# Optimization experiments

Hardware: AMD Instinct MI355X
Metric: run time of the kernel (lower is better)

Reference implementation:

```python
import jax, jax.numpy as jnp
import numpy as np

B, T, D, H, L = 128, 512, 512, 512, 256


def setup_inputs() -> dict:
    key = jax.random.key(0)
    ks = jax.random.split(key, 7)
    lim = 1.0 / np.sqrt(H)
    u = lambda k, shape, lo: jax.random.uniform(k, shape, jnp.float32, -lo, lo)
    x = jax.random.normal(ks[0], (B, T, D), dtype=jnp.float32)
    Wih = u(ks[1], (3 * H, D), lim)
    Whh = u(ks[2], (3 * H, H), lim)
    b = u(ks[3], (3 * H,), lim)
    bn = u(ks[4], (H,), lim)
    lim_l = 1.0 / np.sqrt(H)
    Wlin = u(ks[5], (2 * L, H), lim_l)
    blin = u(ks[6], (2 * L,), lim_l)
    return {"x": x, "Wih": Wih, "Whh": Whh, "b": b, "bn": bn, "Wlin": Wlin, "blin": blin}


def reference(x, Wih, Whh, b, bn, Wlin, blin):
    # x: (B, T, D). Batched GRU recurrence over time via lax.scan.
    def step(h, xt):
        ig = xt @ Wih.T + b           # (B, 3H)
        hg = h @ Whh.T                # (B, 3H)
        ir, iz, inn = jnp.split(ig, 3, axis=-1)
        hr, hz, hn = jnp.split(hg, 3, axis=-1)
        r = jax.nn.sigmoid(ir + hr)
        z = jax.nn.sigmoid(iz + hz)
        n = jnp.tanh(inn + r * (hn + bn))
        h_new = (1.0 - z) * n + z * h
        return h_new, None

    xs = jnp.swapaxes(x, 0, 1)        # (T, B, D)
    h0 = jnp.zeros((x.shape[0], Whh.shape[1]), dtype=x.dtype)
    h_final, _ = jax.lax.scan(step, h0, xs)
    out = h_final @ Wlin.T + blin     # (B, 2L)
    mu, logvar = jnp.split(out, 2, axis=-1)
    return (mu, logvar)
```

## Files before the change

kernel.cpp:

```cpp
#include <hip/hip_runtime.h>
#include <stdint.h>


typedef short short8 __attribute__((ext_vector_type(8)));
typedef float f32x4 __attribute__((ext_vector_type(4)));
typedef int int4v __attribute__((ext_vector_type(4)));

#define NB 128
#define NT 512
#define ND 512
#define NH 512
#define NG 1536
#define HSLOT (NB * NH)

__device__ __forceinline__ unsigned short f2bf(float f) {
  union { float f; unsigned u; } v; v.f = f;
  unsigned r = v.u + 0x7fffu + ((v.u >> 16) & 1u);
  return (unsigned short)(r >> 16);
}
__device__ __forceinline__ float bf2f(unsigned short u) {
  union { unsigned u; float f; } v; v.u = ((unsigned)u) << 16; return v.f;
}
__device__ __forceinline__ float sigmoid_f(float x) {
  float e = __builtin_amdgcn_exp2f(-1.4426950408889634f * x);
  return __builtin_amdgcn_rcpf(1.0f + e);
}
__device__ __forceinline__ float tanh_f(float x) {
  float e = __builtin_amdgcn_exp2f(2.8853900817779268f * x);
  return 1.0f - 2.0f * __builtin_amdgcn_rcpf(1.0f + e);
}
__device__ __forceinline__ short8 pack8(float4 a, float4 b) {
  short8 s;
  s[0] = (short)f2bf(a.x); s[1] = (short)f2bf(a.y);
  s[2] = (short)f2bf(a.z); s[3] = (short)f2bf(a.w);
  s[4] = (short)f2bf(b.x); s[5] = (short)f2bf(b.y);
  s[6] = (short)f2bf(b.z); s[7] = (short)f2bf(b.w);
  return s;
}

__device__ __forceinline__ int4v load16_s(const unsigned short* p) {
  int4v v;
  asm volatile("global_load_dwordx4 %0, %1, off sc0 sc1\n\t"
               "s_waitcnt vmcnt(0)"
               : "=v"(v) : "v"(p) : "memory");
  return v;
}

__device__ __forceinline__ void load16x2_s(const unsigned short* p0,
                                           const unsigned short* p1,
                                           int4v* v0, int4v* v1) {
  asm volatile(
      "global_load_dwordx4 %0, %2, off sc0 sc1\n\t"
      "global_load_dwordx4 %1, %3, off sc0 sc1\n\t"
      "s_waitcnt vmcnt(0)"
      : "=&v"(*v0), "=&v"(*v1) : "v"(p0), "v"(p1) : "memory");
}

__device__ __forceinline__ void store8_nd(unsigned short* p, unsigned long long v) {
  asm volatile("global_store_dwordx2 %0, %1, off sc0 sc1"
               :: "v"(p), "v"(v) : "memory");
}

__device__ __forceinline__ unsigned pkmax(unsigned a, unsigned b) {
  unsigned d;
  asm("v_pk_max_u16 %0, %1, %2" : "=v"(d) : "v"(a), "v"(b));
  return d;
}
__device__ __forceinline__ bool has_sent(int4v v) {
  unsigned m = pkmax(pkmax((unsigned)v[0], (unsigned)v[1]),
                     pkmax((unsigned)v[2], (unsigned)v[3]));
  return ((m & 0xFFFFu) == 0xFFFFu) || ((m >> 16) == 0xFFFFu);
}

__global__ __launch_bounds__(256) void ig_gemm(
    const float* __restrict__ x, const float* __restrict__ Wih,
    const float* __restrict__ bias, unsigned short* __restrict__ IG) {
  __shared__ unsigned short As[128 * 40];
  __shared__ unsigned short Bs[128 * 40];
  const int tid = threadIdx.x;
  const int bn = blockIdx.x, bm = blockIdx.y;
  const int lane = tid & 63, w = tid >> 6;
  const int wm = w >> 1, wn = w & 1;
  const int l15 = lane & 15, q = lane >> 4;

  f32x4 acc[4][4] = {};

  for (int kt = 0; kt < 16; ++kt) {
    __syncthreads();
#pragma unroll
    for (int j = 0; j < 4; ++j) {
      int fi = tid + 256 * j;
      int row = fi >> 3, kq = fi & 7;
      float4 v = *(const float4*)(x + (size_t)(bm * 128 + row) * ND + kt * 32 + kq * 4);
      ushort4 s = {f2bf(v.x), f2bf(v.y), f2bf(v.z), f2bf(v.w)};
      *(ushort4*)&As[row * 40 + kq * 4] = s;
    }
#pragma unroll
    for (int j = 0; j < 4; ++j) {
      int fi = tid + 256 * j;
      int row = fi >> 3, kq = fi & 7;
      float4 v = *(const float4*)(Wih + (size_t)(bn * 128 + row) * ND + kt * 32 + kq * 4);
      ushort4 s = {f2bf(v.x), f2bf(v.y), f2bf(v.z), f2bf(v.w)};
      *(ushort4*)&Bs[row * 40 + kq * 4] = s;
    }
    __syncthreads();

    short8 af[4], bf[4];
#pragma unroll
    for (int tm = 0; tm < 4; ++tm)
      af[tm] = *(const short8*)&As[(wm * 64 + tm * 16 + l15) * 40 + q * 8];
#pragma unroll
    for (int tn = 0; tn < 4; ++tn)
      bf[tn] = *(const short8*)&Bs[(wn * 64 + tn * 16 + l15) * 40 + q * 8];
#pragma unroll
    for (int tm = 0; tm < 4; ++tm)
#pragma unroll
      for (int tn = 0; tn < 4; ++tn)
        acc[tm][tn] = __builtin_amdgcn_mfma_f32_16x16x32_bf16(af[tm], bf[tn], acc[tm][tn], 0, 0, 0);
  }

#pragma unroll
  for (int tm = 0; tm < 4; ++tm) {
#pragma unroll
    for (int tn = 0; tn < 4; ++tn) {
      int col = bn * 128 + wn * 64 + tn * 16 + l15;
      float bb = bias[col];
#pragma unroll
      for (int i = 0; i < 4; ++i) {
        int row = bm * 128 + wm * 64 + tm * 16 + q * 4 + i;
        IG[(size_t)row * NG + col] = f2bf(acc[tm][tn][i] + bb);
      }
    }
  }
}

template <bool USE_IG>
__global__ __launch_bounds__(512, 2) void gru_rec(
    const float* __restrict__ x, const float* __restrict__ Wih,
    const float* __restrict__ Whh, const float* __restrict__ bias,
    const float* __restrict__ bn, const unsigned short* __restrict__ IG,
    unsigned short* __restrict__ hbuf, float* __restrict__ hfin) {
  __shared__ unsigned short hs[16 * 512];
  __shared__ unsigned short ts[16 * 128];

  const int tid = threadIdx.x;
  const int lane = tid & 63;
  const int w = tid >> 6;
  const int l15 = lane & 15, q = lane >> 4;
  const int bid = blockIdx.x;
  const int g = bid & 7, cblk = bid >> 3;
  const int col = cblk * 128 + w * 16 + l15;
  const int erow = g * 16 + q * 4;
  const int mrow = g * 16 + l15;

  short8 bfr[3][16];
#pragma unroll
  for (int gt = 0; gt < 3; ++gt) {
    const float* src = Whh + (size_t)(gt * NH + col) * NH + q * 8;
#pragma unroll
    for (int kk = 0; kk < 16; ++kk) {
      float4 v0 = *(const float4*)(src + kk * 32);
      float4 v1 = *(const float4*)(src + kk * 32 + 4);
      bfr[gt][kk] = pack8(v0, v1);
    }
  }

  float bi_r = 0.f, bi_z = 0.f, bi_n = 0.f;
  if (!USE_IG) {
    bi_r = bias[col];
    bi_z = bias[NH + col];
    bi_n = bias[2 * NH + col];
  }
  const float bnv = bn[col];

  float hreg[4] = {0.f, 0.f, 0.f, 0.f};

  const int frow = tid >> 5;
  const int fsi = (tid & 31) * 2;
  const int fr7 = frow & 7;
  const bool own_slot = ((fsi >> 4) == cblk);

  const int srow = tid >> 5;
  const int scol = (tid & 31) * 4;
  const size_t cell_off = (size_t)(g * 16 + srow) * NH + cblk * 128 + scol;

  for (int t = 0; t < NT; ++t) {
    const unsigned short* hcur = hbuf + (size_t)(t & 3) * HSLOT;
    unsigned short* hnxt  = hbuf + (size_t)((t + 1) & 3) * HSLOT;
    unsigned short* hsent = hbuf + (size_t)((t + 2) & 3) * HSLOT;

    float igr[4], igz[4], ign[4];
    if (USE_IG) {
#pragma unroll
      for (int i = 0; i < 4; ++i) {
        const size_t base = ((size_t)(erow + i) * NT + t) * NG + col;
        igr[i] = bf2f(IG[base]);
        igz[i] = bf2f(IG[base + NH]);
        ign[i] = bf2f(IG[base + 2 * NH]);
      }
    }

    if (t > 0 && own_slot) {
      const int ls0 = (fsi ^ fr7) & 15;
      const int ls1 = ((fsi + 1) ^ fr7) & 15;
      *(int4v*)&hs[frow * 512 + (fsi << 3)] =
          *(const int4v*)&ts[frow * 128 + ls0 * 8];
      *(int4v*)&hs[frow * 512 + ((fsi + 1) << 3)] =
          *(const int4v*)&ts[frow * 128 + ls1 * 8];
    } else {
      const unsigned short* hrow = hcur + (size_t)(g * 16 + frow) * NH;
      const unsigned short* p0 = hrow + ((fsi ^ fr7) << 3);
      const unsigned short* p1 = hrow + (((fsi + 1) ^ fr7) << 3);
      int4v v0, v1;
      load16x2_s(p0, p1, &v0, &v1);
      if (t > 0) {
        while (has_sent(v0)) v0 = load16_s(p0);
        while (has_sent(v1)) v1 = load16_s(p1);
      }
      *(int4v*)&hs[frow * 512 + (fsi << 3)] = v0;
      *(int4v*)&hs[frow * 512 + ((fsi + 1) << 3)] = v1;
    }
    __syncthreads();

    if (t + 2 < NT) {
      store8_nd(hsent + cell_off, 0xFFFFFFFFFFFFFFFFull);
    }

    f32x4 ar = {0.f, 0.f, 0.f, 0.f};
    f32x4 az = {0.f, 0.f, 0.f, 0.f};
    f32x4 an = {0.f, 0.f, 0.f, 0.f};
    f32x4 ai = {0.f, 0.f, 0.f, 0.f};
    const int abase = l15 * 512;
    const int ar7 = (l15 & 7) << 3;
#pragma unroll
    for (int kk = 0; kk < 16; ++kk) {
      short8 afk = *(const short8*)&hs[abase + ((kk * 32 + q * 8) ^ ar7)];
      ar = __builtin_amdgcn_mfma_f32_16x16x32_bf16(afk, bfr[0][kk], ar, 0, 0, 0);
      az = __builtin_amdgcn_mfma_f32_16x16x32_bf16(afk, bfr[1][kk], az, 0, 0, 0);
      an = __builtin_amdgcn_mfma_f32_16x16x32_bf16(afk, bfr[2][kk], an, 0, 0, 0);
      if (!USE_IG) {
        const float* xp = x + ((size_t)mrow * NT + t) * ND + kk * 32 + q * 8;
        short8 xa = pack8(*(const float4*)xp, *(const float4*)(xp + 4));
#pragma unroll
        for (int gt = 0; gt < 3; ++gt) {
          const float* wp = Wih + (size_t)(gt * NH + col) * ND + kk * 32 + q * 8;
          short8 wf = pack8(*(const float4*)wp, *(const float4*)(wp + 4));
          if (gt == 0) ar = __builtin_amdgcn_mfma_f32_16x16x32_bf16(xa, wf, ar, 0, 0, 0);
          if (gt == 1) az = __builtin_amdgcn_mfma_f32_16x16x32_bf16(xa, wf, az, 0, 0, 0);
          if (gt == 2) ai = __builtin_amdgcn_mfma_f32_16x16x32_bf16(xa, wf, ai, 0, 0, 0);
        }
      }
    }

    unsigned short sv[4];
#pragma unroll
    for (int i = 0; i < 4; ++i) {
      float xr = USE_IG ? (ar[i] + igr[i]) : (ar[i] + bi_r);
      float xz = USE_IG ? (az[i] + igz[i]) : (az[i] + bi_z);
      float xin = USE_IG ? ign[i] : (ai[i] + bi_n);
      float r = sigmoid_f(xr);
      float z = sigmoid_f(xz);
      float n = tanh_f(xin + r * (an[i] + bnv));
      float hn2 = (1.f - z) * n + z * hreg[i];
      hreg[i] = hn2;
      sv[i] = f2bf(hn2);
      if (t == NT - 1) hfin[(size_t)(erow + i) * NH + col] = hn2;
    }

    if (t != NT - 1) {
#pragma unroll
      for (int i = 0; i < 4; ++i)
        ts[(q * 4 + i) * 128 + w * 16 + l15] = sv[i];
      asm volatile("s_waitcnt vmcnt(0)" ::: "memory");
      __syncthreads();
      unsigned long long v8 = *(const unsigned long long*)&ts[srow * 128 + scol];
      store8_nd(hnxt + cell_off, v8);
    }
  }
}

__global__ __launch_bounds__(256) void final_linear(
    const float* __restrict__ hfin, const float* __restrict__ Wlin,
    const float* __restrict__ blin, float* __restrict__ out) {
  __shared__ float sh[16 * 516];
  const int tid = threadIdx.x;
  const int b0 = blockIdx.y * 16, o0 = blockIdx.x * 16;

  for (int j = tid; j < 16 * 128; j += 256) {
    int row = j >> 7, kq = j & 127;
    *(float4*)&sh[row * 516 + kq * 4] =
        *(const float4*)(hfin + (size_t)(b0 + row) * NH + kq * 4);
  }
  __syncthreads();

  const int bi = tid & 15, oi = tid >> 4;
  const int o = o0 + oi;
  const float4* wp = (const float4*)(Wlin + (size_t)o * NH);
  float4 a4 = {0.f, 0.f, 0.f, 0.f};
  for (int k4 = 0; k4 < 128; ++k4) {
    float4 wv = wp[k4];
    float4 hv = *(const float4*)&sh[bi * 516 + k4 * 4];
    a4.x += wv.x * hv.x; a4.y += wv.y * hv.y;
    a4.z += wv.z * hv.z; a4.w += wv.w * hv.w;
  }
  float v = a4.x + a4.y + a4.z + a4.w + blin[o];
  int b = b0 + bi;
  if (o < 256) out[b * 256 + o] = v;
  else out[32768 + b * 256 + (o - 256)] = v;
}

extern "C" void kernel_launch(void* const* d_in, const int* in_sizes, int n_in,
                              void* d_out, int out_size, void* d_ws, size_t ws_size,
                              hipStream_t stream) {
  const float* x    = (const float*)d_in[0];
  const float* Wih  = (const float*)d_in[1];
  const float* Whh  = (const float*)d_in[2];
  const float* bias = (const float*)d_in[3];
  const float* bn   = (const float*)d_in[4];
  const float* Wlin = (const float*)d_in[5];
  const float* blin = (const float*)d_in[6];
  float* out = (float*)d_out;

  char* ws = (char*)d_ws;
  unsigned short* hbuf = (unsigned short*)ws;
  float* hfin          = (float*)(ws + 4 * 131072);
  unsigned short* IG   = (unsigned short*)(ws + 4 * 131072 + 262144);
  const size_t need_min = 4 * 131072 + 262144;
  const size_t need_ig  = need_min + (size_t)NB * NT * NG * 2;
  if (ws_size < need_min) return;

  hipMemsetAsync(ws, 0, 131072, stream);
  hipMemsetAsync(ws + 131072, 0xFF, 3 * 131072, stream);

  const bool useIG = (ws_size >= need_ig);
  if (useIG) {
    ig_gemm<<<dim3(12, 512), 256, 0, stream>>>(x, Wih, bias, IG);
    gru_rec<true><<<32, 512, 0, stream>>>(x, Wih, Whh, bias, bn, IG, hbuf, hfin);
  } else {
    gru_rec<false><<<32, 512, 0, stream>>>(x, Wih, Whh, bias, bn, nullptr, hbuf, hfin);
  }
  final_linear<<<dim3(32, 8), 256, 0, stream>>>(hfin, Wlin, blin, out);
}
```

Baseline: 2.186 ms.

## Split GRU recurrence across 64 blocks of 256 threads with narrower column slices

The persistent recurrent kernel moves from 32 blocks of 512 threads (128 hidden columns each) to 64 blocks of 256 threads (64 columns each). The aim is to spread the per-step work and Whh register fragments across more CUs and shorten each block's step. Each thread now fetches four 16-byte chunks of the previous hidden state instead of two, and the transpose staging buffer is halved. In exchange, twice as many blocks take part in the cross-block sentinel handshake every timestep, and each block reads more remote hidden-state data per step.

```diff
diff --git a/kernel.cpp b/kernel.cpp
--- a/kernel.cpp
+++ b/kernel.cpp
@@ -46,14 +46,20 @@
   return v;
 }
 
-__device__ __forceinline__ void load16x2_s(const unsigned short* p0,
+__device__ __forceinline__ void load16x4_s(const unsigned short* p0,
                                            const unsigned short* p1,
-                                           int4v* v0, int4v* v1) {
+                                           const unsigned short* p2,
+                                           const unsigned short* p3,
+                                           int4v* v0, int4v* v1,
+                                           int4v* v2, int4v* v3) {
   asm volatile(
-      "global_load_dwordx4 %0, %2, off sc0 sc1\n\t"
-      "global_load_dwordx4 %1, %3, off sc0 sc1\n\t"
+      "global_load_dwordx4 %0, %4, off sc0 sc1\n\t"
+      "global_load_dwordx4 %1, %5, off sc0 sc1\n\t"
+      "global_load_dwordx4 %2, %6, off sc0 sc1\n\t"
+      "global_load_dwordx4 %3, %7, off sc0 sc1\n\t"
       "s_waitcnt vmcnt(0)"
-      : "=&v"(*v0), "=&v"(*v1) : "v"(p0), "v"(p1) : "memory");
+      : "=&v"(*v0), "=&v"(*v1), "=&v"(*v2), "=&v"(*v3)
+      : "v"(p0), "v"(p1), "v"(p2), "v"(p3) : "memory");
 }
 
 __device__ __forceinline__ void store8_nd(unsigned short* p, unsigned long long v) {
@@ -135,21 +141,21 @@
 }
 
 template <bool USE_IG>
-__global__ __launch_bounds__(512, 2) void gru_rec(
+__global__ __launch_bounds__(256, 1) void gru_rec(
     const float* __restrict__ x, const float* __restrict__ Wih,
     const float* __restrict__ Whh, const float* __restrict__ bias,
     const float* __restrict__ bn, const unsigned short* __restrict__ IG,
     unsigned short* __restrict__ hbuf, float* __restrict__ hfin) {
   __shared__ unsigned short hs[16 * 512];
-  __shared__ unsigned short ts[16 * 128];
+  __shared__ unsigned short ts[16 * 64];
 
   const int tid = threadIdx.x;
   const int lane = tid & 63;
   const int w = tid >> 6;
   const int l15 = lane & 15, q = lane >> 4;
   const int bid = blockIdx.x;
-  const int g = bid & 7, cblk = bid >> 3;
-  const int col = cblk * 128 + w * 16 + l15;
+  const int g = bid & 7, c = bid >> 3;
+  const int col = c * 64 + w * 16 + l15;
   const int erow = g * 16 + q * 4;
   const int mrow = g * 16 + l15;
 
@@ -175,14 +181,14 @@
 
   float hreg[4] = {0.f, 0.f, 0.f, 0.f};
 
-  const int frow = tid >> 5;
-  const int fsi = (tid & 31) * 2;
+  const int frow = tid >> 4;
+  const int fg0 = (tid & 15) * 4;
   const int fr7 = frow & 7;
-  const bool own_slot = ((fsi >> 4) == cblk);
-
-  const int srow = tid >> 5;
-  const int scol = (tid & 31) * 4;
-  const size_t cell_off = (size_t)(g * 16 + srow) * NH + cblk * 128 + scol;
+  const bool own_slot = ((fg0 >> 3) == c);
+
+  const int srow = tid >> 4;
+  const int scol = (tid & 15) * 4;
+  const size_t cell_off = (size_t)(g * 16 + srow) * NH + c * 64 + scol;
 
   for (int t = 0; t < NT; ++t) {
     const unsigned short* hcur = hbuf + (size_t)(t & 3) * HSLOT;
@@ -201,24 +207,31 @@
     }
 
     if (t > 0 && own_slot) {
-      const int ls0 = (fsi ^ fr7) & 15;
-      const int ls1 = ((fsi + 1) ^ fr7) & 15;
-      *(int4v*)&hs[frow * 512 + (fsi << 3)] =
-          *(const int4v*)&ts[frow * 128 + ls0 * 8];
-      *(int4v*)&hs[frow * 512 + ((fsi + 1) << 3)] =
-          *(const int4v*)&ts[frow * 128 + ls1 * 8];
+#pragma unroll
+      for (int j = 0; j < 4; ++j) {
+        const int s = fg0 + j;
+        const int ls = (s ^ fr7) & 7;
+        *(int4v*)&hs[frow * 512 + (s << 3)] =
+            *(const int4v*)&ts[frow * 64 + ls * 8];
+      }
     } else {
       const unsigned short* hrow = hcur + (size_t)(g * 16 + frow) * NH;
-      const unsigned short* p0 = hrow + ((fsi ^ fr7) << 3);
-      const unsigned short* p1 = hrow + (((fsi + 1) ^ fr7) << 3);
-      int4v v0, v1;
-      load16x2_s(p0, p1, &v0, &v1);
+      const unsigned short* p0 = hrow + (((fg0 + 0) ^ fr7) << 3);
+      const unsigned short* p1 = hrow + (((fg0 + 1) ^ fr7) << 3);
+      const unsigned short* p2 = hrow + (((fg0 + 2) ^ fr7) << 3);
+      const unsigned short* p3 = hrow + (((fg0 + 3) ^ fr7) << 3);
+      int4v v0, v1, v2, v3;
+      load16x4_s(p0, p1, p2, p3, &v0, &v1, &v2, &v3);
       if (t > 0) {
         while (has_sent(v0)) v0 = load16_s(p0);
         while (has_sent(v1)) v1 = load16_s(p1);
-      }
-      *(int4v*)&hs[frow * 512 + (fsi << 3)] = v0;
-      *(int4v*)&hs[frow * 512 + ((fsi + 1) << 3)] = v1;
+        while (has_sent(v2)) v2 = load16_s(p2);
+        while (has_sent(v3)) v3 = load16_s(p3);
+      }
+      *(int4v*)&hs[frow * 512 + ((fg0 + 0) << 3)] = v0;
+      *(int4v*)&hs[frow * 512 + ((fg0 + 1) << 3)] = v1;
+      *(int4v*)&hs[frow * 512 + ((fg0 + 2) << 3)] = v2;
+      *(int4v*)&hs[frow * 512 + ((fg0 + 3) << 3)] = v3;
     }
     __syncthreads();
 
@@ -270,10 +283,10 @@
     if (t != NT - 1) {
 #pragma unroll
       for (int i = 0; i < 4; ++i)
-        ts[(q * 4 + i) * 128 + w * 16 + l15] = sv[i];
+        ts[(q * 4 + i) * 64 + w * 16 + l15] = sv[i];
       asm volatile("s_waitcnt vmcnt(0)" ::: "memory");
       __syncthreads();
-      unsigned long long v8 = *(const unsigned long long*)&ts[srow * 128 + scol];
+      unsigned long long v8 = *(const unsigned long long*)&ts[srow * 64 + scol];
       store8_nd(hnxt + cell_off, v8);
     }
   }
@@ -335,9 +348,9 @@
   const bool useIG = (ws_size >= need_ig);
   if (useIG) {
     ig_gemm<<<dim3(12, 512), 256, 0, stream>>>(x, Wih, bias, IG);
-    gru_rec<true><<<32, 512, 0, stream>>>(x, Wih, Whh, bias, bn, IG, hbuf, hfin);
+    gru_rec<true><<<64, 256, 0, stream>>>(x, Wih, Whh, bias, bn, IG, hbuf, hfin);
   } else {
-    gru_rec<false><<<32, 512, 0, stream>>>(x, Wih, Whh, bias, bn, nullptr, hbuf, hfin);
+    gru_rec<false><<<64, 256, 0, stream>>>(x, Wih, Whh, bias, bn, nullptr, hbuf, hfin);
   }
   final_linear<<<dim3(32, 8), 256, 0, stream>>>(hfin, Wlin, blin, out);
 }
```

Measured after the change: 2.079 ms. 1.05x faster.
